# Kernel optimization log

Hardware: AMD Instinct MI355X
Metric: run time of the kernel (lower is better)

Reference implementation:

```python
import jax, jax.numpy as jnp
import numpy as np

B, S, H, F, E, K = 8, 4096, 256, 512, 16, 2
EPS = 1e-5


def setup_inputs() -> dict:
    key = jax.random.key(0)
    ks = jax.random.split(key, 9)
    sc = 0.02
    return {
        "x": jax.random.normal(ks[0], (B, S, H), dtype=jnp.float32),
        "gate_w": jax.random.normal(ks[1], (H, E), dtype=jnp.float32) * sc,
        "gate_b": jnp.zeros((E,), dtype=jnp.float32),
        "w1": jax.random.normal(ks[2], (E, H, F), dtype=jnp.float32) * sc,
        "b1": jnp.zeros((E, F), dtype=jnp.float32),
        "w2": jax.random.normal(ks[3], (E, F, H), dtype=jnp.float32) * sc,
        "b2": jnp.zeros((E, H), dtype=jnp.float32),
        "gamma": jnp.ones((H,), dtype=jnp.float32),
        "beta": jnp.zeros((H,), dtype=jnp.float32),
    }


def reference(x, gate_w, gate_b, w1, b1, w2, b2, gamma, beta):
    # gating: top-k over expert logits, softmax over the k selected logits
    gate_logits = x @ gate_w + gate_b                      # [B,S,E]
    topk_vals, topk_idx = jax.lax.top_k(gate_logits, K)    # [B,S,K]
    topk_w = jax.nn.softmax(topk_vals, axis=-1)            # [B,S,K]

    # naive dense MoE: every expert runs over every token (matches source)
    h = jax.nn.relu(jnp.einsum('bsh,ehf->bsef', x, w1) + b1)   # [B,S,E,F]
    expert_out = jnp.einsum('bsef,efh->bseh', h, w2) + b2       # [B,S,E,H]

    # select top-k expert outputs and combine with gate weights
    sel = jnp.take_along_axis(expert_out, topk_idx[:, :, :, None], axis=2)  # [B,S,K,H]
    moe = jnp.sum(topk_w[..., None] * sel, axis=2)              # [B,S,H]

    # residual + LayerNorm
    y = x + moe
    mu = jnp.mean(y, axis=-1, keepdims=True)
    var = jnp.var(y, axis=-1, keepdims=True)
    return (y - mu) / jnp.sqrt(var + EPS) * gamma + beta
```

## Files before the change

### kernel.cpp

```cpp
#include <hip/hip_runtime.h>
#include <hip/hip_bf16.h>

typedef __bf16 bf16_t;
typedef __bf16 bf16x8 __attribute__((ext_vector_type(8)));
typedef __bf16 bf16x4 __attribute__((ext_vector_type(4)));
typedef float f32x4 __attribute__((ext_vector_type(4)));

#define NB 8
#define NS 4096
#define NH 256
#define NF 512
#define NE 16
#define NTOK (NB*NS)
#define TT 64
#define NCH 16
#define XS_STRIDE 264
#define HS_STRIDE 40

__global__ __launch_bounds__(256) void transpose_kernel(
    const float* __restrict__ w1, const float* __restrict__ w2,
    bf16_t* __restrict__ w1t, bf16_t* __restrict__ w2t)
{
    __shared__ float tile[32][33];
    int bid = blockIdx.x;
    const float* src; bf16_t* dst; int R, C; int isw1;
    if (bid < 2048) { src = w1; dst = w1t; R = NH; C = NF; isw1 = 1; }
    else            { bid -= 2048; src = w2; dst = w2t; R = NF; C = NH; isw1 = 0; }
    const int tilesPerE = 128;
    int e = bid / tilesPerE;
    int t = bid % tilesPerE;
    int tcols = C / 32;
    int tr = (t / tcols) * 32, tc = (t % tcols) * 32;
    src += (size_t)e * R * C;
    dst += (size_t)e * R * C;
    int tx = threadIdx.x & 31, ty0 = threadIdx.x >> 5;
    #pragma unroll
    for (int i = 0; i < 4; i++) {
        int ty = ty0 + i * 8;
        tile[ty][tx] = src[(size_t)(tr + ty) * C + tc + tx];
    }
    __syncthreads();
    #pragma unroll
    for (int i = 0; i < 4; i++) {
        int ty = ty0 + i * 8;
        int drow = tc + ty;
        int dcol = tr + tx;
        size_t idx;
        if (isw1) {
            int swz = (((dcol >> 3) ^ (drow & 7)) << 3) | (dcol & 7);
            idx = (size_t)drow * NH + swz;
        } else {
            idx = (size_t)drow * R + dcol;
        }
        dst[idx] = (bf16_t)tile[tx][ty];
    }
}

__global__ __launch_bounds__(256) void gate_kernel(
    const float* __restrict__ x, const float* __restrict__ gate_w,
    const float* __restrict__ gate_b,
    int* __restrict__ counts, int* __restrict__ bucket_enc,
    float* __restrict__ bucket_gw, bf16_t* __restrict__ xb)
{
    __shared__ float gws[NH][NE];
    __shared__ int lcnt[NE];
    __shared__ int gbase[NE];

    for (int i = threadIdx.x; i < NH * NE; i += 256)
        gws[i >> 4][i & 15] = gate_w[i];
    if (threadIdx.x < NE) lcnt[threadIdx.x] = 0;
    __syncthreads();

    int   pe[2][2];
    int   po[2][2];
    float pg[2][2];
    int   toks[2];

    #pragma unroll
    for (int t = 0; t < 2; t++) {
        int tok = blockIdx.x * 512 + t * 256 + threadIdx.x;
        toks[t] = tok;
        const float4* xr = (const float4*)(x + (size_t)tok * NH);
        bf16x4* xbr = (bf16x4*)(xb + (size_t)tok * NH);
        float acc[NE];
        #pragma unroll
        for (int e = 0; e < NE; e++) acc[e] = gate_b[e];
        for (int h4 = 0; h4 < NH / 4; h4++) {
            float4 xv = xr[h4];
            bf16x4 xo;
            xo[0] = (bf16_t)xv.x; xo[1] = (bf16_t)xv.y;
            xo[2] = (bf16_t)xv.z; xo[3] = (bf16_t)xv.w;
            xbr[h4] = xo;
            #pragma unroll
            for (int j = 0; j < 4; j++) {
                float xs = (j == 0) ? xv.x : (j == 1) ? xv.y : (j == 2) ? xv.z : xv.w;
                int h = h4 * 4 + j;
                #pragma unroll
                for (int e = 0; e < NE; e++) acc[e] += xs * gws[h][e];
            }
        }
        float v0 = -1e30f, v1 = -1e30f; int i0 = 0, i1 = 0;
        #pragma unroll
        for (int e = 0; e < NE; e++) {
            float a = acc[e];
            if (a > v0)      { v1 = v0; i1 = i0; v0 = a; i0 = e; }
            else if (a > v1) { v1 = a; i1 = e; }
        }
        float e1 = __expf(v1 - v0);
        float s  = 1.f + e1;
        pe[t][0] = i0; pe[t][1] = i1;
        pg[t][0] = 1.f / s; pg[t][1] = e1 / s;
        po[t][0] = atomicAdd(&lcnt[i0], 1);
        po[t][1] = atomicAdd(&lcnt[i1], 1);
    }
    __syncthreads();
    if (threadIdx.x < NE)
        gbase[threadIdx.x] = atomicAdd(&counts[threadIdx.x], lcnt[threadIdx.x]);
    __syncthreads();
    #pragma unroll
    for (int t = 0; t < 2; t++)
        #pragma unroll
        for (int k = 0; k < 2; k++) {
            int e = pe[t][k];
            int pos = gbase[e] + po[t][k];
            bucket_enc[e * NTOK + pos] = toks[t] | (k << 20);
            bucket_gw [e * NTOK + pos] = pg[t][k];
        }
}

__global__ __launch_bounds__(256, 2) void moe_kernel(
    const bf16_t* __restrict__ xb,
    const bf16_t* __restrict__ w1t,
    const float*  __restrict__ b1,
    const bf16_t* __restrict__ w2t,
    const float*  __restrict__ b2,
    const int* __restrict__ counts,
    const int* __restrict__ bucket_enc,
    const float* __restrict__ bucket_gw,
    bf16_t* __restrict__ pairbuf)
{
    __shared__ __align__(16) bf16_t Xs[TT][XS_STRIDE];
    __shared__ uint4 W1s4[2][1024];
    __shared__ __align__(16) bf16_t Hs[2][TT][HS_STRIDE];
    __shared__ int   tok_s[TT];
    __shared__ float gw_s[TT];

    int flat = blockIdx.x;
    int e     = (flat & 7) * 2 + ((flat >> 3) & 1);
    int tile0 = flat >> 4;
    int n_e = counts[e];
    int wave = threadIdx.x >> 6;
    int lane = threadIdx.x & 63;
    int l15 = lane & 15, q = lane >> 4;

    const bf16_t* w1te = w1t + (size_t)e * NF * NH;
    const bf16_t* w2te = w2t + (size_t)e * NH * NF;

    int ntiles = (n_e + TT - 1) / TT;
    for (int tile = tile0; tile < ntiles; tile += 64) {
        int tstart = tile * TT;
        __syncthreads();
        if (threadIdx.x < TT) {
            int slot = tstart + threadIdx.x;
            if (slot < n_e) {
                tok_s[threadIdx.x] = bucket_enc[e * NTOK + slot];
                gw_s [threadIdx.x] = bucket_gw [e * NTOK + slot];
            } else { tok_s[threadIdx.x] = 0; gw_s[threadIdx.x] = 0.f; }
        }
        __syncthreads();
        {
            int c  = threadIdx.x & 31;
            int r0 = threadIdx.x >> 5;
            #pragma unroll
            for (int i = 0; i < 8; i++) {
                int r = r0 + i * 8;
                int tok = tok_s[r] & 0xFFFFF;
                const uint4* src = (const uint4*)(xb + (size_t)tok * NH) + c;
                *(uint4*)&Xs[r][c * 8] = *src;
            }
            const uint4* gw1 = (const uint4*)w1te;
            #pragma unroll
            for (int i = 0; i < 4; i++)
                W1s4[0][i * 256 + threadIdx.x] = gw1[i * 256 + threadIdx.x];
        }
        __syncthreads();

        f32x4 oacc[4][4];
        #pragma unroll
        for (int a = 0; a < 4; a++)
            #pragma unroll
            for (int b = 0; b < 4; b++) { f32x4 z = {0.f,0.f,0.f,0.f}; oacc[a][b] = z; }

        for (int ch = 0; ch < NCH; ch++) {
            int buf = ch & 1;
            uint4 pf[4];
            bool do_pf = (ch + 1 < NCH);
            if (do_pf) {
                const uint4* gw1 = (const uint4*)(w1te + (size_t)(ch + 1) * 32 * NH);
                #pragma unroll
                for (int i = 0; i < 4; i++) pf[i] = gw1[i * 256 + threadIdx.x];
            }
            bf16x8 bf2[4];
            #pragma unroll
            for (int nt = 0; nt < 4; nt++) {
                int hh = wave * 64 + nt * 16 + l15;
                bf2[nt] = *(const bf16x8*)&w2te[(size_t)hh * NF + ch * 32 + q * 8];
            }
            f32x4 hacc[2]; { f32x4 z = {0.f,0.f,0.f,0.f}; hacc[0] = z; hacc[1] = z; }
            const bf16_t* w1s = (const bf16_t*)W1s4[buf];
            #pragma unroll
            for (int ks = 0; ks < NH / 32; ks++) {
                bf16x8 afrag = *(const bf16x8*)&Xs[wave * 16 + l15][ks * 32 + q * 8];
                #pragma unroll
                for (int n = 0; n < 2; n++) {
                    int fl = n * 16 + l15;
                    bf16x8 bfrag = *(const bf16x8*)&w1s[fl * NH + ((((ks * 4 + q) ^ (fl & 7))) << 3)];
                    hacc[n] = __builtin_amdgcn_mfma_f32_16x16x32_bf16(afrag, bfrag, hacc[n], 0, 0, 0);
                }
            }
            #pragma unroll
            for (int n = 0; n < 2; n++) {
                int f = ch * 32 + n * 16 + l15;
                float bv = b1[e * NF + f];
                #pragma unroll
                for (int r = 0; r < 4; r++) {
                    float v = hacc[n][r] + bv;
                    v = v > 0.f ? v : 0.f;
                    Hs[buf][wave * 16 + q * 4 + r][n * 16 + l15] = (bf16_t)v;
                }
            }
            if (do_pf) {
                #pragma unroll
                for (int i = 0; i < 4; i++)
                    W1s4[buf ^ 1][i * 256 + threadIdx.x] = pf[i];
            }
            __syncthreads();
            #pragma unroll
            for (int mt = 0; mt < 4; mt++) {
                bf16x8 afrag = *(const bf16x8*)&Hs[buf][mt * 16 + l15][q * 8];
                #pragma unroll
                for (int nt = 0; nt < 4; nt++) {
                    oacc[mt][nt] = __builtin_amdgcn_mfma_f32_16x16x32_bf16(afrag, bf2[nt], oacc[mt][nt], 0, 0, 0);
                }
            }
        }
        #pragma unroll
        for (int nt = 0; nt < 4; nt++) {
            int col = wave * 64 + nt * 16 + l15;
            float b2v = b2[e * NH + col];
            #pragma unroll
            for (int mt = 0; mt < 4; mt++) {
                #pragma unroll
                for (int r = 0; r < 4; r++) {
                    int row = mt * 16 + q * 4 + r;
                    if (tstart + row < n_e) {
                        int enc = tok_s[row];
                        int tok = enc & 0xFFFFF;
                        int k   = enc >> 20;
                        float v = (oacc[mt][nt][r] + b2v) * gw_s[row];
                        pairbuf[((size_t)(tok * 2 + k)) * NH + col] = (bf16_t)v;
                    }
                }
            }
        }
    }
}

__global__ __launch_bounds__(256) void ln_kernel(
    const float* __restrict__ x, const bf16_t* __restrict__ pairbuf,
    const float* __restrict__ gamma, const float* __restrict__ beta,
    float* __restrict__ out)
{
    int tok = blockIdx.x;
    int h = threadIdx.x;
    float y = x[(size_t)tok * NH + h]
            + (float)pairbuf[(size_t)(tok * 2) * NH + h]
            + (float)pairbuf[(size_t)(tok * 2 + 1) * NH + h];
    float s = y, s2 = y * y;
    #pragma unroll
    for (int o = 32; o > 0; o >>= 1) { s += __shfl_down(s, o); s2 += __shfl_down(s2, o); }
    __shared__ float red[8];
    int wave = threadIdx.x >> 6, lane = threadIdx.x & 63;
    if (lane == 0) { red[wave] = s; red[4 + wave] = s2; }
    __syncthreads();
    if (threadIdx.x == 0) {
        float ts  = red[0] + red[1] + red[2] + red[3];
        float ts2 = red[4] + red[5] + red[6] + red[7];
        float mu  = ts / NH;
        float var = ts2 / NH - mu * mu;
        red[0] = mu;
        red[1] = rsqrtf(var + 1e-5f);
    }
    __syncthreads();
    float mu = red[0], rstd = red[1];
    out[(size_t)tok * NH + h] = ((y - mu) * rstd) * gamma[h] + beta[h];
}

extern "C" void kernel_launch(void* const* d_in, const int* in_sizes, int n_in,
                              void* d_out, int out_size, void* d_ws, size_t ws_size,
                              hipStream_t stream) {
    const float* x      = (const float*)d_in[0];
    const float* gate_w = (const float*)d_in[1];
    const float* gate_b = (const float*)d_in[2];
    const float* w1     = (const float*)d_in[3];
    const float* b1     = (const float*)d_in[4];
    const float* w2     = (const float*)d_in[5];
    const float* b2     = (const float*)d_in[6];
    const float* gamma  = (const float*)d_in[7];
    const float* beta   = (const float*)d_in[8];
    float* out = (float*)d_out;

    char* ws = (char*)d_ws;
    const size_t MB = 1024 * 1024;
    int*    counts     = (int*)ws;
    int*    bucket_enc = (int*)(ws + 256);
    float*  bucket_gw  = (float*)(ws + 256 + 2 * MB);
    bf16_t* w1t        = (bf16_t*)(ws + 256 + 4 * MB);
    bf16_t* w2t        = (bf16_t*)(ws + 256 + 8 * MB);
    bf16_t* xb         = (bf16_t*)(ws + 256 + 12 * MB);
    bf16_t* pairbuf    = (bf16_t*)(ws + 256 + 28 * MB);

    hipMemsetAsync(counts, 0, 256, stream);
    transpose_kernel<<<4096, 256, 0, stream>>>(w1, w2, w1t, w2t);
    gate_kernel<<<64, 256, 0, stream>>>(x, gate_w, gate_b, counts, bucket_enc, bucket_gw, xb);
    moe_kernel<<<1024, 256, 0, stream>>>(xb, w1t, b1, w2t, b2, counts, bucket_enc, bucket_gw, pairbuf);
    ln_kernel<<<NTOK, 256, 0, stream>>>(x, pairbuf, gamma, beta, out);
}
```

Baseline: 280.8 us.

## Swizzle LDS tiles, block w2 layout, stage MoE output, vectorize LN and transpose

```diff
diff --git a/kernel.cpp b/kernel.cpp
--- a/kernel.cpp
+++ b/kernel.cpp
@@ -14,8 +14,9 @@
 #define NTOK (NB*NS)
 #define TT 64
 #define NCH 16
-#define XS_STRIDE 264
-#define HS_STRIDE 40
+
+#define XS_U(r,u) (((r) << 5) + ((u) ^ ((r) & 7)))
+#define HS_U(r,u) (((r) << 2) + ((u) ^ (((r) >> 2) & 3)))
 
 __global__ __launch_bounds__(256) void transpose_kernel(
     const float* __restrict__ w1, const float* __restrict__ w2,
@@ -26,9 +27,8 @@
     const float* src; bf16_t* dst; int R, C; int isw1;
     if (bid < 2048) { src = w1; dst = w1t; R = NH; C = NF; isw1 = 1; }
     else            { bid -= 2048; src = w2; dst = w2t; R = NF; C = NH; isw1 = 0; }
-    const int tilesPerE = 128;
-    int e = bid / tilesPerE;
-    int t = bid % tilesPerE;
+    int e = bid >> 7;
+    int t = bid & 127;
     int tcols = C / 32;
     int tr = (t / tcols) * 32, tc = (t % tcols) * 32;
     src += (size_t)e * R * C;
@@ -40,19 +40,24 @@
         tile[ty][tx] = src[(size_t)(tr + ty) * C + tc + tx];
     }
     __syncthreads();
-    #pragma unroll
-    for (int i = 0; i < 4; i++) {
-        int ty = ty0 + i * 8;
-        int drow = tc + ty;
-        int dcol = tr + tx;
+    if (threadIdx.x < 128) {
+        int j = threadIdx.x & 31;
+        int g = threadIdx.x >> 5;
+        bf16x8 v;
+        #pragma unroll
+        for (int jj = 0; jj < 8; jj++)
+            v[jj] = (bf16_t)tile[g * 8 + jj][j];
         size_t idx;
         if (isw1) {
-            int swz = (((dcol >> 3) ^ (drow & 7)) << 3) | (dcol & 7);
-            idx = (size_t)drow * NH + swz;
+            int f  = tc + j;
+            int kb = tr + g * 8;
+            idx = (size_t)f * NH + ((((kb >> 3) ^ (f & 7))) << 3);
         } else {
-            idx = (size_t)drow * R + dcol;
-        }
-        dst[idx] = (bf16_t)tile[tx][ty];
+            int h  = tc + j;
+            int fb = tr + g * 8;
+            idx = ((size_t)(fb >> 5) * NH + h) * 32 + (fb & 31);
+        }
+        *(bf16x8*)(dst + idx) = v;
     }
 }
 
@@ -71,61 +76,51 @@
     if (threadIdx.x < NE) lcnt[threadIdx.x] = 0;
     __syncthreads();
 
-    int   pe[2][2];
-    int   po[2][2];
-    float pg[2][2];
-    int   toks[2];
-
-    #pragma unroll
-    for (int t = 0; t < 2; t++) {
-        int tok = blockIdx.x * 512 + t * 256 + threadIdx.x;
-        toks[t] = tok;
-        const float4* xr = (const float4*)(x + (size_t)tok * NH);
-        bf16x4* xbr = (bf16x4*)(xb + (size_t)tok * NH);
-        float acc[NE];
+    int tok = blockIdx.x * 256 + threadIdx.x;
+    const float4* xr = (const float4*)(x + (size_t)tok * NH);
+    bf16x4* xbr = (bf16x4*)(xb + (size_t)tok * NH);
+    float acc[NE];
+    #pragma unroll
+    for (int e = 0; e < NE; e++) acc[e] = gate_b[e];
+    for (int h4 = 0; h4 < NH / 4; h4++) {
+        float4 xv = xr[h4];
+        bf16x4 xo;
+        xo[0] = (bf16_t)xv.x; xo[1] = (bf16_t)xv.y;
+        xo[2] = (bf16_t)xv.z; xo[3] = (bf16_t)xv.w;
+        xbr[h4] = xo;
         #pragma unroll
-        for (int e = 0; e < NE; e++) acc[e] = gate_b[e];
-        for (int h4 = 0; h4 < NH / 4; h4++) {
-            float4 xv = xr[h4];
-            bf16x4 xo;
-            xo[0] = (bf16_t)xv.x; xo[1] = (bf16_t)xv.y;
-            xo[2] = (bf16_t)xv.z; xo[3] = (bf16_t)xv.w;
-            xbr[h4] = xo;
-            #pragma unroll
-            for (int j = 0; j < 4; j++) {
-                float xs = (j == 0) ? xv.x : (j == 1) ? xv.y : (j == 2) ? xv.z : xv.w;
-                int h = h4 * 4 + j;
-                #pragma unroll
-                for (int e = 0; e < NE; e++) acc[e] += xs * gws[h][e];
-            }
-        }
-        float v0 = -1e30f, v1 = -1e30f; int i0 = 0, i1 = 0;
-        #pragma unroll
-        for (int e = 0; e < NE; e++) {
-            float a = acc[e];
-            if (a > v0)      { v1 = v0; i1 = i0; v0 = a; i0 = e; }
-            else if (a > v1) { v1 = a; i1 = e; }
-        }
-        float e1 = __expf(v1 - v0);
-        float s  = 1.f + e1;
-        pe[t][0] = i0; pe[t][1] = i1;
-        pg[t][0] = 1.f / s; pg[t][1] = e1 / s;
-        po[t][0] = atomicAdd(&lcnt[i0], 1);
-        po[t][1] = atomicAdd(&lcnt[i1], 1);
-    }
+        for (int j = 0; j < 4; j++) {
+            float xs = (j == 0) ? xv.x : (j == 1) ? xv.y : (j == 2) ? xv.z : xv.w;
+            int h = h4 * 4 + j;
+            #pragma unroll
+            for (int e = 0; e < NE; e++) acc[e] += xs * gws[h][e];
+        }
+    }
+    float v0 = -1e30f, v1 = -1e30f; int i0 = 0, i1 = 0;
+    #pragma unroll
+    for (int e = 0; e < NE; e++) {
+        float a = acc[e];
+        if (a > v0)      { v1 = v0; i1 = i0; v0 = a; i0 = e; }
+        else if (a > v1) { v1 = a; i1 = e; }
+    }
+    float e1 = __expf(v1 - v0);
+    float s  = 1.f + e1;
+    int   pe[2] = { i0, i1 };
+    float pg[2] = { 1.f / s, e1 / s };
+    int   po[2];
+    po[0] = atomicAdd(&lcnt[i0], 1);
+    po[1] = atomicAdd(&lcnt[i1], 1);
     __syncthreads();
     if (threadIdx.x < NE)
         gbase[threadIdx.x] = atomicAdd(&counts[threadIdx.x], lcnt[threadIdx.x]);
     __syncthreads();
     #pragma unroll
-    for (int t = 0; t < 2; t++)
-        #pragma unroll
-        for (int k = 0; k < 2; k++) {
-            int e = pe[t][k];
-            int pos = gbase[e] + po[t][k];
-            bucket_enc[e * NTOK + pos] = toks[t] | (k << 20);
-            bucket_gw [e * NTOK + pos] = pg[t][k];
-        }
+    for (int k = 0; k < 2; k++) {
+        int e = pe[k];
+        int pos = gbase[e] + po[k];
+        bucket_enc[e * NTOK + pos] = tok | (k << 20);
+        bucket_gw [e * NTOK + pos] = pg[k];
+    }
 }
 
 __global__ __launch_bounds__(256, 2) void moe_kernel(
@@ -139,9 +134,9 @@
     const float* __restrict__ bucket_gw,
     bf16_t* __restrict__ pairbuf)
 {
-    __shared__ __align__(16) bf16_t Xs[TT][XS_STRIDE];
+    __shared__ uint4 Xs4[TT * 32];
     __shared__ uint4 W1s4[2][1024];
-    __shared__ __align__(16) bf16_t Hs[2][TT][HS_STRIDE];
+    __shared__ uint4 Hs4[2][TT * 4];
     __shared__ int   tok_s[TT];
     __shared__ float gw_s[TT];
 
@@ -154,7 +149,7 @@
     int l15 = lane & 15, q = lane >> 4;
 
     const bf16_t* w1te = w1t + (size_t)e * NF * NH;
-    const bf16_t* w2te = w2t + (size_t)e * NH * NF;
+    const bf16_t* w2te = w2t + (size_t)e * NF * NH;
 
     int ntiles = (n_e + TT - 1) / TT;
     for (int tile = tile0; tile < ntiles; tile += 64) {
@@ -175,8 +170,7 @@
             for (int i = 0; i < 8; i++) {
                 int r = r0 + i * 8;
                 int tok = tok_s[r] & 0xFFFFF;
-                const uint4* src = (const uint4*)(xb + (size_t)tok * NH) + c;
-                *(uint4*)&Xs[r][c * 8] = *src;
+                Xs4[XS_U(r, c)] = ((const uint4*)(xb + (size_t)tok * NH))[c];
             }
             const uint4* gw1 = (const uint4*)w1te;
             #pragma unroll
@@ -196,7 +190,7 @@
             uint4 pf[4];
             bool do_pf = (ch + 1 < NCH);
             if (do_pf) {
-                const uint4* gw1 = (const uint4*)(w1te + (size_t)(ch + 1) * 32 * NH);
+                const uint4* gw1 = (const uint4*)w1te + (size_t)(ch + 1) * 1024;
                 #pragma unroll
                 for (int i = 0; i < 4; i++) pf[i] = gw1[i * 256 + threadIdx.x];
             }
@@ -204,13 +198,14 @@
             #pragma unroll
             for (int nt = 0; nt < 4; nt++) {
                 int hh = wave * 64 + nt * 16 + l15;
-                bf2[nt] = *(const bf16x8*)&w2te[(size_t)hh * NF + ch * 32 + q * 8];
+                bf2[nt] = *(const bf16x8*)&w2te[(((size_t)ch * NH + hh) << 5) + q * 8];
             }
             f32x4 hacc[2]; { f32x4 z = {0.f,0.f,0.f,0.f}; hacc[0] = z; hacc[1] = z; }
             const bf16_t* w1s = (const bf16_t*)W1s4[buf];
-            #pragma unroll
-            for (int ks = 0; ks < NH / 32; ks++) {
-                bf16x8 afrag = *(const bf16x8*)&Xs[wave * 16 + l15][ks * 32 + q * 8];
+            __builtin_amdgcn_s_setprio(1);
+            #pragma unroll
+            for (int ks = 0; ks < 8; ks++) {
+                bf16x8 afrag = *(const bf16x8*)&Xs4[XS_U(wave * 16 + l15, ks * 4 + q)];
                 #pragma unroll
                 for (int n = 0; n < 2; n++) {
                     int fl = n * 16 + l15;
@@ -218,15 +213,20 @@
                     hacc[n] = __builtin_amdgcn_mfma_f32_16x16x32_bf16(afrag, bfrag, hacc[n], 0, 0, 0);
                 }
             }
-            #pragma unroll
-            for (int n = 0; n < 2; n++) {
-                int f = ch * 32 + n * 16 + l15;
-                float bv = b1[e * NF + f];
-                #pragma unroll
-                for (int r = 0; r < 4; r++) {
-                    float v = hacc[n][r] + bv;
-                    v = v > 0.f ? v : 0.f;
-                    Hs[buf][wave * 16 + q * 4 + r][n * 16 + l15] = (bf16_t)v;
+            __builtin_amdgcn_s_setprio(0);
+            {
+                bf16_t* hsb = (bf16_t*)Hs4[buf];
+                #pragma unroll
+                for (int n = 0; n < 2; n++) {
+                    int f = ch * 32 + n * 16 + l15;
+                    float bv = b1[e * NF + f];
+                    #pragma unroll
+                    for (int r = 0; r < 4; r++) {
+                        float v = hacc[n][r] + bv;
+                        v = v > 0.f ? v : 0.f;
+                        int row = wave * 16 + q * 4 + r;
+                        hsb[row * 32 + ((n * 16 + l15) ^ (((row >> 2) & 3) << 3))] = (bf16_t)v;
+                    }
                 }
             }
             if (do_pf) {
@@ -235,31 +235,47 @@
                     W1s4[buf ^ 1][i * 256 + threadIdx.x] = pf[i];
             }
             __syncthreads();
+            __builtin_amdgcn_s_setprio(1);
             #pragma unroll
             for (int mt = 0; mt < 4; mt++) {
-                bf16x8 afrag = *(const bf16x8*)&Hs[buf][mt * 16 + l15][q * 8];
+                bf16x8 afrag = *(const bf16x8*)&Hs4[buf][HS_U(mt * 16 + l15, q)];
                 #pragma unroll
                 for (int nt = 0; nt < 4; nt++) {
                     oacc[mt][nt] = __builtin_amdgcn_mfma_f32_16x16x32_bf16(afrag, bf2[nt], oacc[mt][nt], 0, 0, 0);
                 }
             }
-        }
-        #pragma unroll
-        for (int nt = 0; nt < 4; nt++) {
-            int col = wave * 64 + nt * 16 + l15;
-            float b2v = b2[e * NH + col];
-            #pragma unroll
-            for (int mt = 0; mt < 4; mt++) {
-                #pragma unroll
-                for (int r = 0; r < 4; r++) {
-                    int row = mt * 16 + q * 4 + r;
-                    if (tstart + row < n_e) {
-                        int enc = tok_s[row];
-                        int tok = enc & 0xFFFFF;
-                        int k   = enc >> 20;
+            __builtin_amdgcn_s_setprio(0);
+        }
+        {
+            bf16_t* xsb = (bf16_t*)Xs4;
+            #pragma unroll
+            for (int nt = 0; nt < 4; nt++) {
+                int col = wave * 64 + nt * 16 + l15;
+                float b2v = b2[e * NH + col];
+                #pragma unroll
+                for (int mt = 0; mt < 4; mt++) {
+                    #pragma unroll
+                    for (int r = 0; r < 4; r++) {
+                        int row = mt * 16 + q * 4 + r;
                         float v = (oacc[mt][nt][r] + b2v) * gw_s[row];
-                        pairbuf[((size_t)(tok * 2 + k)) * NH + col] = (bf16_t)v;
+                        xsb[row * NH + (col ^ ((row & 7) << 3))] = (bf16_t)v;
                     }
+                }
+            }
+        }
+        __syncthreads();
+        {
+            int nrows = n_e - tstart; if (nrows > TT) nrows = TT;
+            int c  = threadIdx.x & 31;
+            int r0 = threadIdx.x >> 5;
+            #pragma unroll
+            for (int i = 0; i < 8; i++) {
+                int r = r0 + i * 8;
+                if (r < nrows) {
+                    int enc = tok_s[r];
+                    int tok = enc & 0xFFFFF;
+                    int k   = enc >> 20;
+                    ((uint4*)(pairbuf + ((size_t)(tok * 2 + k)) * NH))[c] = Xs4[XS_U(r, c)];
                 }
             }
         }
@@ -271,29 +287,33 @@
     const float* __restrict__ gamma, const float* __restrict__ beta,
     float* __restrict__ out)
 {
-    int tok = blockIdx.x;
-    int h = threadIdx.x;
-    float y = x[(size_t)tok * NH + h]
-            + (float)pairbuf[(size_t)(tok * 2) * NH + h]
-            + (float)pairbuf[(size_t)(tok * 2 + 1) * NH + h];
-    float s = y, s2 = y * y;
-    #pragma unroll
-    for (int o = 32; o > 0; o >>= 1) { s += __shfl_down(s, o); s2 += __shfl_down(s2, o); }
-    __shared__ float red[8];
-    int wave = threadIdx.x >> 6, lane = threadIdx.x & 63;
-    if (lane == 0) { red[wave] = s; red[4 + wave] = s2; }
-    __syncthreads();
-    if (threadIdx.x == 0) {
-        float ts  = red[0] + red[1] + red[2] + red[3];
-        float ts2 = red[4] + red[5] + red[6] + red[7];
-        float mu  = ts / NH;
-        float var = ts2 / NH - mu * mu;
-        red[0] = mu;
-        red[1] = rsqrtf(var + 1e-5f);
-    }
-    __syncthreads();
-    float mu = red[0], rstd = red[1];
-    out[(size_t)tok * NH + h] = ((y - mu) * rstd) * gamma[h] + beta[h];
+    int tok  = blockIdx.x * 4 + (threadIdx.x >> 6);
+    int lane = threadIdx.x & 63;
+    float4 xv = *(const float4*)(x + (size_t)tok * NH + lane * 4);
+    bf16x4 p0 = *(const bf16x4*)(pairbuf + (size_t)(tok * 2)     * NH + lane * 4);
+    bf16x4 p1 = *(const bf16x4*)(pairbuf + (size_t)(tok * 2 + 1) * NH + lane * 4);
+    float y0 = xv.x + (float)p0[0] + (float)p1[0];
+    float y1 = xv.y + (float)p0[1] + (float)p1[1];
+    float y2 = xv.z + (float)p0[2] + (float)p1[2];
+    float y3 = xv.w + (float)p0[3] + (float)p1[3];
+    float s  = y0 + y1 + y2 + y3;
+    float s2 = y0 * y0 + y1 * y1 + y2 * y2 + y3 * y3;
+    #pragma unroll
+    for (int o = 32; o > 0; o >>= 1) {
+        s  += __shfl_xor(s, o);
+        s2 += __shfl_xor(s2, o);
+    }
+    float mu   = s * (1.f / NH);
+    float var  = s2 * (1.f / NH) - mu * mu;
+    float rstd = rsqrtf(var + 1e-5f);
+    float4 gv = *(const float4*)(gamma + lane * 4);
+    float4 bv = *(const float4*)(beta  + lane * 4);
+    float4 o4;
+    o4.x = (y0 - mu) * rstd * gv.x + bv.x;
+    o4.y = (y1 - mu) * rstd * gv.y + bv.y;
+    o4.z = (y2 - mu) * rstd * gv.z + bv.z;
+    o4.w = (y3 - mu) * rstd * gv.w + bv.w;
+    *(float4*)(out + (size_t)tok * NH + lane * 4) = o4;
 }
 
 extern "C" void kernel_launch(void* const* d_in, const int* in_sizes, int n_in,
@@ -322,7 +342,7 @@
 
     hipMemsetAsync(counts, 0, 256, stream);
     transpose_kernel<<<4096, 256, 0, stream>>>(w1, w2, w1t, w2t);
-    gate_kernel<<<64, 256, 0, stream>>>(x, gate_w, gate_b, counts, bucket_enc, bucket_gw, xb);
+    gate_kernel<<<128, 256, 0, stream>>>(x, gate_w, gate_b, counts, bucket_enc, bucket_gw, xb);
     moe_kernel<<<1024, 256, 0, stream>>>(xb, w1t, b1, w2t, b2, counts, bucket_enc, bucket_gw, pairbuf);
-    ln_kernel<<<NTOK, 256, 0, stream>>>(x, pairbuf, gamma, beta, out);
-}
+    ln_kernel<<<NTOK / 4, 256, 0, stream>>>(x, pairbuf, gamma, beta, out);
+}
```

After: 266.1 us. 1.06x faster.
